# Kernel optimization log

Measured on AMD Instinct MI355X. Metric: run time of the kernel, lower is better.

Reference implementation:

```python
import jax, jax.numpy as jnp
import numpy as np

B, L, D, H = 2, 2048, 2048, 16
Dh = D // H
EPS = 1e-6
THETA = 500000.0


def _rope_cos_sin(dh, seq_len):
    # matches init_rope: per-head dim, theta=500000
    inv_freqs = 1.0 / (THETA ** (jnp.arange(0, dh, 2, dtype=jnp.float32) / dh))  # [Dh/2]
    t = jnp.arange(seq_len, dtype=jnp.float32)
    freqs = jnp.outer(t, inv_freqs)  # [L, Dh/2]
    return jnp.cos(freqs), jnp.sin(freqs)


def _apply_rope(x, cos, sin):
    # x: [B,L,H,Dh]; cos/sin: [L,Dh/2]
    xr = x.reshape(*x.shape[:-1], -1, 2)  # [B,L,H,Dh/2,2]
    c = cos[None, :, None, :]
    s = sin[None, :, None, :]
    rot = jnp.stack([xr[..., 0] * c - xr[..., 1] * s,
                     xr[..., 1] * c + xr[..., 0] * s], axis=-1)
    return rot.reshape(x.shape)


def setup_inputs() -> dict:
    key = jax.random.key(0)
    ks = jax.random.split(key, 5)
    std = 0.02
    x = jax.random.normal(ks[0], (B, L, D), dtype=jnp.float32)
    Wq = std * jax.random.normal(ks[1], (D, H, Dh), dtype=jnp.float32)
    Wk = std * jax.random.normal(ks[2], (D, H, Dh), dtype=jnp.float32)
    Wv = std * jax.random.normal(ks[3], (D, H, Dh), dtype=jnp.float32)
    Wout = (std / jnp.sqrt(2.0 * 24)) * jax.random.normal(ks[4], (D, D), dtype=jnp.float32)
    attn_scale = jnp.asarray(jnp.log2(float(L) ** 2 - float(L)), dtype=jnp.float32)
    return {"x": x, "Wq": Wq, "Wk": Wk, "Wv": Wv, "Wout": Wout, "attn_scale": attn_scale}


def reference(x, Wq, Wk, Wv, Wout, attn_scale):
    cos, sin = _rope_cos_sin(Dh, L)
    q = jnp.einsum('bld,dhk->blhk', x, Wq)  # [B,L,H,Dh]
    k = jnp.einsum('bld,dhk->blhk', x, Wk)
    v = jnp.einsum('bld,dhk->blhk', x, Wv)
    q = _apply_rope(q, cos, sin)
    k = _apply_rope(k, cos, sin)
    # QK L2 normalization
    q = q / (jnp.linalg.norm(q, axis=-1, keepdims=True) + EPS)
    k = k / (jnp.linalg.norm(k, axis=-1, keepdims=True) + EPS)
    att = jnp.einsum('bqhd,bkhd->bhqk', q, k)  # [B,H,L,L]
    mask = jnp.tril(jnp.ones((1, 1, L, L), dtype=jnp.bool_))
    neg_inf = jnp.finfo(jnp.float32).min
    att = jnp.where(mask, att, neg_inf)
    att = attn_scale * att
    att = jax.nn.softmax(att, axis=-1)
    out = jnp.einsum('bhqk,bkhd->bqhd', att, v)  # [B,L,H,Dh]
    out = out.reshape(B, L, D)
    return jnp.einsum('bld,de->ble', out, Wout)
```

## Files before the change

### kernel.cpp

```cpp
#include <hip/hip_runtime.h>
#include <hip/hip_fp16.h>

#define B_ 2
#define L_ 2048
#define D_ 2048
#define H_ 16
#define DH_ 128

typedef _Float16 f16;
typedef _Float16 f16x8 __attribute__((ext_vector_type(8)));
typedef _Float16 f16x4 __attribute__((ext_vector_type(4)));
typedef _Float16 f16x2 __attribute__((ext_vector_type(2)));
typedef float f32x4 __attribute__((ext_vector_type(4)));

__device__ __forceinline__ void gload_lds16(const void* g, void* l) {
  __builtin_amdgcn_global_load_lds(
      (__attribute__((address_space(1))) void*)(void*)g,
      (__attribute__((address_space(3))) void*)l, 16, 0, 0);
}

__device__ __forceinline__ float rmax16(float v) {
  v = fmaxf(v, __shfl_xor(v, 1));
  v = fmaxf(v, __shfl_xor(v, 2));
  v = fmaxf(v, __shfl_xor(v, 4));
  v = fmaxf(v, __shfl_xor(v, 8));
  return v;
}
__device__ __forceinline__ float rsum16(float v) {
  v += __shfl_xor(v, 1);
  v += __shfl_xor(v, 2);
  v += __shfl_xor(v, 4);
  v += __shfl_xor(v, 8);
  return v;
}

__global__ __launch_bounds__(256) void k_cast(const float* __restrict__ in,
                                              f16* __restrict__ out, int n8) {
  int i = blockIdx.x * blockDim.x + threadIdx.x;
  if (i >= n8) return;
  const float4* p = (const float4*)in + (size_t)i * 2;
  float4 a = p[0], b = p[1];
  f16x8 o;
  o[0] = (f16)a.x; o[1] = (f16)a.y; o[2] = (f16)a.z; o[3] = (f16)a.w;
  o[4] = (f16)b.x; o[5] = (f16)b.y; o[6] = (f16)b.z; o[7] = (f16)b.w;
  *((f16x8*)out + i) = o;
}

__global__ __launch_bounds__(256) void k_transpose4(
    const float* __restrict__ W0, const float* __restrict__ W1,
    const float* __restrict__ W2, const float* __restrict__ W3,
    f16* __restrict__ T0, f16* __restrict__ T1, f16* __restrict__ T2,
    f16* __restrict__ T3) {
  int z = blockIdx.z;
  const float* src = (z == 0) ? W0 : (z == 1) ? W1 : (z == 2) ? W2 : W3;
  f16* dst = (z == 0) ? T0 : (z == 1) ? T1 : (z == 2) ? T2 : T3;
  __shared__ float tile[32][33];
  int tx = threadIdx.x, ty = threadIdx.y;
  int x = blockIdx.x * 32 + tx;
  int y0 = blockIdx.y * 32;
#pragma unroll
  for (int i = 0; i < 4; ++i)
    tile[ty + i * 8][tx] = src[(size_t)(y0 + ty + i * 8) * 2048 + x];
  __syncthreads();
  int ox = y0 + tx;
  int oy0 = blockIdx.x * 32;
#pragma unroll
  for (int i = 0; i < 4; ++i)
    dst[(size_t)(oy0 + ty + i * 8) * 2048 + ox] = (f16)tile[tx][ty + i * 8];
}

__device__ __forceinline__ void gemm_core(const f16* __restrict__ A,
                                          const f16* __restrict__ BT,
                                          f16* As, f16* Bs, int m0, int n0,
                                          f32x4 (&acc)[4][4]) {
  const int tid = threadIdx.x;
  const int lane = tid & 63, w = tid >> 6;
  const int wr = w >> 1, wc = w & 1;
  const int li = lane & 15, lg = lane >> 4;
  for (int kt = 0; kt < 64; ++kt) {
    __syncthreads();
#pragma unroll
    for (int p = 0; p < 2; ++p) {
      int o = tid * 16 + p * 4096;
      int row = o >> 6, cb = o & 63;
      gload_lds16((const char*)A + (size_t)(m0 + row) * 4096 + kt * 64 + cb,
                  (char*)As + o);
      gload_lds16((const char*)BT + (size_t)(n0 + row) * 4096 + kt * 64 + cb,
                  (char*)Bs + o);
    }
    __syncthreads();
    f16x8 af[4], bf[4];
#pragma unroll
    for (int i = 0; i < 4; ++i) {
      af[i] = *(const f16x8*)(As + (wr * 64 + i * 16 + li) * 32 + lg * 8);
      bf[i] = *(const f16x8*)(Bs + (wc * 64 + i * 16 + li) * 32 + lg * 8);
    }
#pragma unroll
    for (int i = 0; i < 4; ++i)
#pragma unroll
      for (int j = 0; j < 4; ++j)
        acc[i][j] =
            __builtin_amdgcn_mfma_f32_16x16x32_f16(af[i], bf[j], acc[i][j], 0, 0, 0);
  }
}

__global__ __launch_bounds__(256) void k_gemm_qkv(
    const f16* __restrict__ x16, const f16* __restrict__ WqT,
    const f16* __restrict__ WkT, const f16* __restrict__ WvT,
    f16* __restrict__ qh, f16* __restrict__ kh, f16* __restrict__ vTo) {
  __shared__ alignas(16) f16 As[128 * 32];
  __shared__ alignas(16) f16 Bs[128 * 32];
  const int z = blockIdx.z;
  const f16* BT = (z == 0) ? WqT : (z == 1) ? WkT : WvT;
  const int m0 = blockIdx.y * 128, n0 = blockIdx.x * 128;
  f32x4 acc[4][4] = {};
  gemm_core(x16, BT, As, Bs, m0, n0, acc);
  const int lane = threadIdx.x & 63, w = threadIdx.x >> 6;
  const int wr = w >> 1, wc = w & 1, li = lane & 15, lg = lane >> 4;
  if (z < 2) {
    f16* out = (z == 0) ? qh : kh;
#pragma unroll
    for (int i = 0; i < 4; ++i) {
      int mb = m0 + wr * 64 + i * 16 + lg * 4;
#pragma unroll
      for (int j = 0; j < 4; ++j) {
        int n = n0 + wc * 64 + j * 16 + li;
        int h = n >> 7, dh = n & 127;
#pragma unroll
        for (int r = 0; r < 4; ++r) {
          int m = mb + r;
          int b = m >> 11, l = m & 2047;
          out[(((size_t)(b * 16 + h) * 2048 + l) << 7) + dh] = (f16)acc[i][j][r];
        }
      }
    }
  } else {
#pragma unroll
    for (int i = 0; i < 4; ++i) {
      int mb = m0 + wr * 64 + i * 16 + lg * 4;
      int b = mb >> 11, l = mb & 2047;
#pragma unroll
      for (int j = 0; j < 4; ++j) {
        int n = n0 + wc * 64 + j * 16 + li;
        int h = n >> 7, dh = n & 127;
        f16x4 v4;
#pragma unroll
        for (int r = 0; r < 4; ++r) v4[r] = (f16)acc[i][j][r];
        *(f16x4*)(vTo + ((size_t)(b * 16 + h) * 128 + dh) * 2048 + l) = v4;
      }
    }
  }
}

__global__ __launch_bounds__(256) void k_rope_norm(f16* __restrict__ qh,
                                                   f16* __restrict__ kh) {
  int gid = blockIdx.x * 4 + (threadIdx.x >> 6);
  int lane = threadIdx.x & 63;
  int which = gid >> 16;
  int r = gid & 65535;
  int l = r & 2047;
  f16* base = (which ? kh : qh) + (size_t)r * 128;
  f16x2 xv = *(f16x2*)(base + lane * 2);
  float x0 = (float)xv[0], x1 = (float)xv[1];
  float invf = exp2f(-(float)lane * 0.29580575889569f);
  float ang = (float)l * invf;
  float s, c;
  sincosf(ang, &s, &c);
  float y0 = x0 * c - x1 * s;
  float y1 = x1 * c + x0 * s;
  float ss = y0 * y0 + y1 * y1;
  ss += __shfl_xor(ss, 1);  ss += __shfl_xor(ss, 2);
  ss += __shfl_xor(ss, 4);  ss += __shfl_xor(ss, 8);
  ss += __shfl_xor(ss, 16); ss += __shfl_xor(ss, 32);
  float inv = 1.0f / (sqrtf(ss) + 1e-6f);
  f16x2 o;
  o[0] = (f16)(y0 * inv);
  o[1] = (f16)(y1 * inv);
  *(f16x2*)(base + lane * 2) = o;
}

__global__ __launch_bounds__(256) void k_flash(
    const f16* __restrict__ qh, const f16* __restrict__ kh,
    const f16* __restrict__ vT, f16* __restrict__ attO,
    const float* __restrict__ ascale_p) {
  const int bh = blockIdx.y;
  const int tid = threadIdx.x, lane = tid & 63, w = tid >> 6;
  const int li = lane & 15, lg = lane >> 4;
  const float csc = ascale_p[0] * 1.44269504088896f;
  const float thr = 8.0f / csc;

  __shared__ alignas(16) f16 Ks[64 * 136];
  __shared__ alignas(16) f16 Vs[128 * 72];
  __shared__ alignas(16) f16 Ps[4][16 * 72];

  const f16* qb = qh + (size_t)bh * 2048 * 128;
  const f16* kb = kh + (size_t)bh * 2048 * 128;
  const f16* vb = vT + (size_t)bh * 128 * 2048;
  const int b = bh >> 4, h = bh & 15;

#pragma unroll 1
  for (int ti = 0; ti < 2; ++ti) {
    const int t = ti ? (31 - (int)blockIdx.x) : (int)blockIdx.x;
    const int qw = t * 64 + w * 16;

    f16x8 Qr[4];
#pragma unroll
    for (int ks = 0; ks < 4; ++ks)
      Qr[ks] = *(const f16x8*)(qb + (size_t)(qw + li) * 128 + ks * 32 + lg * 8);

    f32x4 Oa[8] = {};
    float mrow[4], lrow[4];
#pragma unroll
    for (int r = 0; r < 4; ++r) { mrow[r] = -1e30f; lrow[r] = 0.0f; }

#pragma unroll 1
    for (int kt = 0; kt <= t; ++kt) {
      const int k0 = kt * 64;
      __syncthreads();
#pragma unroll
      for (int p = 0; p < 4; ++p) {
        int e = (p * 256 + tid) * 8;
        int row = e >> 7, col = e & 127;
        *(f16x8*)(Ks + row * 136 + col) =
            *(const f16x8*)(kb + (size_t)(k0 + row) * 128 + col);
        int row2 = e >> 6, col2 = e & 63;
        *(f16x8*)(Vs + row2 * 72 + col2) =
            *(const f16x8*)(vb + (size_t)row2 * 2048 + k0 + col2);
      }
      __syncthreads();

      f32x4 Sa[4] = {};
      __builtin_amdgcn_s_setprio(1);
#pragma unroll
      for (int ks = 0; ks < 4; ++ks) {
        f16x8 kf4[4];
#pragma unroll
        for (int kf = 0; kf < 4; ++kf)
          kf4[kf] = *(const f16x8*)(Ks + (kf * 16 + li) * 136 + ks * 32 + lg * 8);
#pragma unroll
        for (int kf = 0; kf < 4; ++kf)
          Sa[kf] = __builtin_amdgcn_mfma_f32_16x16x32_f16(Qr[ks], kf4[kf],
                                                          Sa[kf], 0, 0, 0);
      }
      __builtin_amdgcn_s_setprio(0);

      if (kt == t) {
#pragma unroll
        for (int kf = 0; kf < 4; ++kf)
#pragma unroll
          for (int r = 0; r < 4; ++r) {
            int qq = qw + lg * 4 + r;
            int kk = k0 + kf * 16 + li;
            if (kk > qq) Sa[kf][r] = -1e30f;
          }
      }

      float vmax[4];
      bool need = false;
#pragma unroll
      for (int r = 0; r < 4; ++r) {
        float v = fmaxf(fmaxf(Sa[0][r], Sa[1][r]), fmaxf(Sa[2][r], Sa[3][r]));
        v = rmax16(v);
        vmax[r] = v;
        need |= (v > mrow[r] + thr);
      }
      if (__any(need)) {
#pragma unroll
        for (int r = 0; r < 4; ++r) {
          float mnew = fmaxf(mrow[r], vmax[r]);
          float sc = exp2f(csc * (mrow[r] - mnew));
          mrow[r] = mnew;
          lrow[r] *= sc;
#pragma unroll
          for (int df = 0; df < 8; ++df) Oa[df][r] *= sc;
        }
      }
#pragma unroll
      for (int r = 0; r < 4; ++r) {
        float rs = 0.0f;
#pragma unroll
        for (int kf = 0; kf < 4; ++kf) {
          float p = exp2f(csc * (Sa[kf][r] - mrow[r]));
          Sa[kf][r] = p;
          rs += p;
        }
        rs = rsum16(rs);
        lrow[r] += rs;
      }

      f16* Pw = &Ps[w][0];
#pragma unroll
      for (int kf = 0; kf < 4; ++kf)
#pragma unroll
        for (int r = 0; r < 4; ++r)
          Pw[(lg * 4 + r) * 72 + kf * 16 + li] = (f16)Sa[kf][r];
      asm volatile("s_waitcnt lgkmcnt(0)" ::: "memory");
      __builtin_amdgcn_sched_barrier(0);
      __builtin_amdgcn_s_setprio(1);
#pragma unroll
      for (int k2 = 0; k2 < 2; ++k2) {
        f16x8 pa, vfr[8];
        pa = *(const f16x8*)(Pw + li * 72 + k2 * 32 + lg * 8);
#pragma unroll
        for (int df = 0; df < 8; ++df)
          vfr[df] = *(const f16x8*)(Vs + (df * 16 + li) * 72 + k2 * 32 + lg * 8);
#pragma unroll
        for (int df = 0; df < 8; ++df)
          Oa[df] = __builtin_amdgcn_mfma_f32_16x16x32_f16(pa, vfr[df],
                                                          Oa[df], 0, 0, 0);
      }
      __builtin_amdgcn_s_setprio(0);
    }

#pragma unroll
    for (int r = 0; r < 4; ++r) {
      float inv = 1.0f / lrow[r];
      int q = qw + lg * 4 + r;
      f16* orow = attO + (size_t)(b * 2048 + q) * 2048 + h * 128;
#pragma unroll
      for (int df = 0; df < 8; ++df)
        orow[df * 16 + li] = (f16)(Oa[df][r] * inv);
    }
  }
}

__global__ __launch_bounds__(256) void k_gemm_out(const f16* __restrict__ A,
                                                  const f16* __restrict__ WoutT,
                                                  float* __restrict__ out) {
  __shared__ alignas(16) f16 As[128 * 32];
  __shared__ alignas(16) f16 Bs[128 * 32];
  const int m0 = blockIdx.y * 128, n0 = blockIdx.x * 128;
  f32x4 acc[4][4] = {};
  gemm_core(A, WoutT, As, Bs, m0, n0, acc);
  const int lane = threadIdx.x & 63, w = threadIdx.x >> 6;
  const int wr = w >> 1, wc = w & 1, li = lane & 15, lg = lane >> 4;
#pragma unroll
  for (int i = 0; i < 4; ++i)
#pragma unroll
    for (int j = 0; j < 4; ++j) {
      int n = n0 + wc * 64 + j * 16 + li;
#pragma unroll
      for (int r = 0; r < 4; ++r) {
        int m = m0 + wr * 64 + i * 16 + lg * 4 + r;
        out[(size_t)m * 2048 + n] = acc[i][j][r];
      }
    }
}

extern "C" void kernel_launch(void* const* d_in, const int* in_sizes, int n_in,
                              void* d_out, int out_size, void* d_ws, size_t ws_size,
                              hipStream_t stream) {
  (void)in_sizes; (void)n_in; (void)out_size; (void)ws_size;
  const float* x = (const float*)d_in[0];
  const float* Wq = (const float*)d_in[1];
  const float* Wk = (const float*)d_in[2];
  const float* Wv = (const float*)d_in[3];
  const float* Wout = (const float*)d_in[4];
  const float* ascale = (const float*)d_in[5];

  char* ws = (char*)d_ws;
  f16* x16 = (f16*)(ws);
  f16* WoutT = (f16*)(ws + (16ull << 20));
  f16* WqT = (f16*)(ws + (24ull << 20));
  f16* WkT = (f16*)(ws + (32ull << 20));
  f16* WvT = (f16*)(ws + (40ull << 20));
  f16* qh = (f16*)(ws + (48ull << 20));
  f16* kh = (f16*)(ws + (64ull << 20));
  f16* vT = (f16*)(ws + (80ull << 20));
  f16* attO = (f16*)(ws + (24ull << 20));

  k_cast<<<dim3(4096), dim3(256), 0, stream>>>(x, x16, 1048576);
  k_transpose4<<<dim3(64, 64, 4), dim3(32, 8), 0, stream>>>(Wq, Wk, Wv, Wout,
                                                            WqT, WkT, WvT, WoutT);
  k_gemm_qkv<<<dim3(16, 32, 3), dim3(256), 0, stream>>>(x16, WqT, WkT, WvT, qh, kh, vT);
  k_rope_norm<<<dim3(32768), dim3(256), 0, stream>>>(qh, kh);
  k_flash<<<dim3(16, 32), dim3(256), 0, stream>>>(qh, kh, vT, attO, ascale);
  k_gemm_out<<<dim3(16, 32), dim3(256), 0, stream>>>(attO, WoutT, (float*)d_out);
}
```

Measured before the change: 441.6 us.

## Replace GEMM core with double-buffered 8-wave swizzled-LDS pipelined kernel

Both projection GEMMs move to a new 512-thread core with larger tiles (256x256 for QKV, 128x256 for the output projection) and a K-step of 64. It double-buffers LDS with XOR-swizzled layout and issues global-to-LDS prefetches interleaved with the MFMA phases. Waits use explicit vmcnt, and block indices are remapped to group tiles for cache locality. The goal is to hide global load latency, cut LDS bank conflicts and raise MFMA utilisation, at the cost of more registers and LDS, fewer blocks, and fragile hand-written wait counts.

```diff
diff --git a/kernel.cpp b/kernel.cpp
--- a/kernel.cpp
+++ b/kernel.cpp
@@ -17,6 +17,14 @@
   __builtin_amdgcn_global_load_lds(
       (__attribute__((address_space(1))) void*)(void*)g,
       (__attribute__((address_space(3))) void*)l, 16, 0, 0);
+}
+
+template <int N>
+__device__ __forceinline__ void waitcnt_vm() {
+  if constexpr (N == 0) asm volatile("s_waitcnt vmcnt(0)" ::: "memory");
+  else if constexpr (N == 4) asm volatile("s_waitcnt vmcnt(4)" ::: "memory");
+  else if constexpr (N == 6) asm volatile("s_waitcnt vmcnt(6)" ::: "memory");
+  else if constexpr (N == 8) asm volatile("s_waitcnt vmcnt(8)" ::: "memory");
 }
 
 __device__ __forceinline__ float rmax16(float v) {
@@ -69,84 +77,184 @@
     dst[(size_t)(oy0 + ty + i * 8) * 2048 + ox] = (f16)tile[tx][ty + i * 8];
 }
 
-__device__ __forceinline__ void gemm_core(const f16* __restrict__ A,
-                                          const f16* __restrict__ BT,
-                                          f16* As, f16* Bs, int m0, int n0,
-                                          f32x4 (&acc)[4][4]) {
+
+template <int NL>
+__device__ __forceinline__ void stage_slot(const char* __restrict__ src,
+                                           char* dst, int tid) {
+#pragma unroll
+  for (int j = 0; j < NL; ++j) {
+    int ci = j * 512 + tid;
+    int row = ci >> 3;
+    int sc = (ci & 7) ^ (row & 7);
+    gload_lds16(src + (size_t)row * 4096 + sc * 16, dst + ci * 16);
+  }
+}
+
+template <int BM>
+__device__ __forceinline__ void gemm8_core(const f16* __restrict__ A,
+                                           const f16* __restrict__ BT,
+                                           char* lds, int m0, int n0,
+                                           f32x4 (&acc)[BM / 32][4]) {
+  constexpr int WRS = BM / 2;
+  constexpr int MR = BM / 32;
+  constexpr int MPP = MR / 4;
+  constexpr int ALOADS = BM / 128;
+  constexpr int LPT = 2 * ALOADS + 4;
+  constexpr int ABYTES = BM * 128;
+  constexpr int BUFB = ABYTES + 32768;
+  constexpr int nt = 32;
+
   const int tid = threadIdx.x;
   const int lane = tid & 63, w = tid >> 6;
-  const int wr = w >> 1, wc = w & 1;
+  const int wr = w >> 2, wc = w & 3;
   const int li = lane & 15, lg = lane >> 4;
-  for (int kt = 0; kt < 64; ++kt) {
-    __syncthreads();
-#pragma unroll
-    for (int p = 0; p < 2; ++p) {
-      int o = tid * 16 + p * 4096;
-      int row = o >> 6, cb = o & 63;
-      gload_lds16((const char*)A + (size_t)(m0 + row) * 4096 + kt * 64 + cb,
-                  (char*)As + o);
-      gload_lds16((const char*)BT + (size_t)(n0 + row) * 4096 + kt * 64 + cb,
-                  (char*)Bs + o);
-    }
-    __syncthreads();
-    f16x8 af[4], bf[4];
-#pragma unroll
-    for (int i = 0; i < 4; ++i) {
-      af[i] = *(const f16x8*)(As + (wr * 64 + i * 16 + li) * 32 + lg * 8);
-      bf[i] = *(const f16x8*)(Bs + (wc * 64 + i * 16 + li) * 32 + lg * 8);
-    }
-#pragma unroll
-    for (int i = 0; i < 4; ++i)
-#pragma unroll
-      for (int j = 0; j < 4; ++j)
-        acc[i][j] =
-            __builtin_amdgcn_mfma_f32_16x16x32_f16(af[i], bf[j], acc[i][j], 0, 0, 0);
-  }
-}
-
-__global__ __launch_bounds__(256) void k_gemm_qkv(
+
+  const char* Ab = (const char*)A + (size_t)m0 * 4096;
+  const char* Bb = (const char*)BT + (size_t)n0 * 4096;
+
+  const int aoff0 = (wr * WRS + li) * 128 + ((lg) ^ (li & 7)) * 16;
+  const int aoff1 = (wr * WRS + li) * 128 + ((4 + lg) ^ (li & 7)) * 16;
+  const int boff0 = (wc * 64 + li) * 128 + ((lg) ^ (li & 7)) * 16;
+  const int boff1 = (wc * 64 + li) * 128 + ((4 + lg) ^ (li & 7)) * 16;
+
+#pragma unroll
+  for (int t = 0; t < 2; ++t) {
+    char* bA = lds + t * BUFB;
+    stage_slot<ALOADS>(Ab + t * 128, bA, tid);
+    stage_slot<ALOADS>(Ab + (size_t)WRS * 4096 + t * 128, bA + (size_t)WRS * 128, tid);
+    stage_slot<2>(Bb + t * 128, bA + ABYTES, tid);
+    stage_slot<2>(Bb + (size_t)128 * 4096 + t * 128, bA + ABYTES + 128 * 128, tid);
+  }
+  waitcnt_vm<LPT>();
+  __builtin_amdgcn_s_barrier();
+
+#pragma unroll 1
+  for (int u = 0; u < nt; ++u) {
+    const int c = u & 1;
+    char* bufA = lds + c * BUFB;
+    char* bufB = bufA + ABYTES;
+    char* oA = lds + (c ^ 1) * BUFB;
+    f16x8 bf[4][2];
+#pragma unroll
+    for (int p = 0; p < 4; ++p) {
+      f16x8 af[MPP][2];
+#pragma unroll
+      for (int i = 0; i < MPP; ++i) {
+        af[i][0] = *(const f16x8*)(bufA + aoff0 + (p * MPP + i) * 2048);
+        af[i][1] = *(const f16x8*)(bufA + aoff1 + (p * MPP + i) * 2048);
+      }
+      if (p == 0) {
+#pragma unroll
+        for (int nc = 0; nc < 4; ++nc) {
+          bf[nc][0] = *(const f16x8*)(bufB + boff0 + nc * 2048);
+          bf[nc][1] = *(const f16x8*)(bufB + boff1 + nc * 2048);
+        }
+      }
+      if (p == 0 && u >= 1 && u + 1 < nt)
+        stage_slot<ALOADS>(Ab + (size_t)(u + 1) * 128, oA, tid);
+      if (p == 1 && u >= 1 && u + 1 < nt)
+        stage_slot<ALOADS>(Ab + (size_t)WRS * 4096 + (size_t)(u + 1) * 128,
+                           oA + (size_t)WRS * 128, tid);
+      if (p == 2 && u + 2 < nt)
+        stage_slot<2>(Bb + (size_t)(u + 2) * 128, bufB, tid);
+      if (p == 3 && u + 2 < nt)
+        stage_slot<2>(Bb + (size_t)128 * 4096 + (size_t)(u + 2) * 128,
+                      bufB + 128 * 128, tid);
+      if (p == 3) {
+        if (u + 2 < nt) waitcnt_vm<4>();
+        else if (u + 1 < nt) waitcnt_vm<0>();
+      }
+      __builtin_amdgcn_s_barrier();
+      asm volatile("s_waitcnt lgkmcnt(0)" ::: "memory");
+      __builtin_amdgcn_sched_barrier(0);
+      __builtin_amdgcn_s_setprio(1);
+#pragma unroll
+      for (int i = 0; i < MPP; ++i)
+#pragma unroll
+        for (int nc = 0; nc < 4; ++nc) {
+          acc[p * MPP + i][nc] = __builtin_amdgcn_mfma_f32_16x16x32_f16(
+              af[i][0], bf[nc][0], acc[p * MPP + i][nc], 0, 0, 0);
+          acc[p * MPP + i][nc] = __builtin_amdgcn_mfma_f32_16x16x32_f16(
+              af[i][1], bf[nc][1], acc[p * MPP + i][nc], 0, 0, 0);
+        }
+      __builtin_amdgcn_s_setprio(0);
+      __builtin_amdgcn_s_barrier();
+    }
+  }
+}
+
+__global__ __launch_bounds__(512, 2) void k_gemm8_qkv(
     const f16* __restrict__ x16, const f16* __restrict__ WqT,
     const f16* __restrict__ WkT, const f16* __restrict__ WvT,
     f16* __restrict__ qh, f16* __restrict__ kh, f16* __restrict__ vTo) {
-  __shared__ alignas(16) f16 As[128 * 32];
-  __shared__ alignas(16) f16 Bs[128 * 32];
-  const int z = blockIdx.z;
+  __shared__ alignas(16) char lds[2 * (256 * 128 + 32768)];
+  const int pb = blockIdx.x;
+  const int lgc = (pb & 7) * 48 + (pb >> 3);
+  const int z = lgc >> 7;
+  const int r = lgc & 127;
+  const int m0 = (r >> 3) * 256, n0 = (r & 7) * 256;
   const f16* BT = (z == 0) ? WqT : (z == 1) ? WkT : WvT;
-  const int m0 = blockIdx.y * 128, n0 = blockIdx.x * 128;
-  f32x4 acc[4][4] = {};
-  gemm_core(x16, BT, As, Bs, m0, n0, acc);
+  f32x4 acc[8][4] = {};
+  gemm8_core<256>(x16, BT, lds, m0, n0, acc);
+
   const int lane = threadIdx.x & 63, w = threadIdx.x >> 6;
-  const int wr = w >> 1, wc = w & 1, li = lane & 15, lg = lane >> 4;
+  const int wr = w >> 2, wc = w & 3, li = lane & 15, lg = lane >> 4;
   if (z < 2) {
     f16* out = (z == 0) ? qh : kh;
 #pragma unroll
-    for (int i = 0; i < 4; ++i) {
-      int mb = m0 + wr * 64 + i * 16 + lg * 4;
-#pragma unroll
-      for (int j = 0; j < 4; ++j) {
-        int n = n0 + wc * 64 + j * 16 + li;
+    for (int mr = 0; mr < 8; ++mr) {
+      int mb = m0 + wr * 128 + mr * 16 + lg * 4;
+#pragma unroll
+      for (int nc = 0; nc < 4; ++nc) {
+        int n = n0 + wc * 64 + nc * 16 + li;
         int h = n >> 7, dh = n & 127;
 #pragma unroll
-        for (int r = 0; r < 4; ++r) {
-          int m = mb + r;
+        for (int r2 = 0; r2 < 4; ++r2) {
+          int m = mb + r2;
           int b = m >> 11, l = m & 2047;
-          out[(((size_t)(b * 16 + h) * 2048 + l) << 7) + dh] = (f16)acc[i][j][r];
+          out[(((size_t)(b * 16 + h) * 2048 + l) << 7) + dh] = (f16)acc[mr][nc][r2];
         }
       }
     }
   } else {
 #pragma unroll
-    for (int i = 0; i < 4; ++i) {
-      int mb = m0 + wr * 64 + i * 16 + lg * 4;
+    for (int mr = 0; mr < 8; ++mr) {
+      int mb = m0 + wr * 128 + mr * 16 + lg * 4;
       int b = mb >> 11, l = mb & 2047;
 #pragma unroll
-      for (int j = 0; j < 4; ++j) {
-        int n = n0 + wc * 64 + j * 16 + li;
+      for (int nc = 0; nc < 4; ++nc) {
+        int n = n0 + wc * 64 + nc * 16 + li;
         int h = n >> 7, dh = n & 127;
         f16x4 v4;
 #pragma unroll
-        for (int r = 0; r < 4; ++r) v4[r] = (f16)acc[i][j][r];
+        for (int r2 = 0; r2 < 4; ++r2) v4[r2] = (f16)acc[mr][nc][r2];
         *(f16x4*)(vTo + ((size_t)(b * 16 + h) * 128 + dh) * 2048 + l) = v4;
+      }
+    }
+  }
+}
+
+__global__ __launch_bounds__(512, 2) void k_gemm8_out(
+    const f16* __restrict__ A, const f16* __restrict__ WoutT,
+    float* __restrict__ out) {
+  __shared__ alignas(16) char lds[2 * (128 * 128 + 32768)];
+  const int pb = blockIdx.x;
+  const int lgc = (pb & 7) * 32 + (pb >> 3);
+  const int m0 = (lgc >> 3) * 128, n0 = (lgc & 7) * 256;
+  f32x4 acc[4][4] = {};
+  gemm8_core<128>(A, WoutT, lds, m0, n0, acc);
+
+  const int lane = threadIdx.x & 63, w = threadIdx.x >> 6;
+  const int wr = w >> 2, wc = w & 3, li = lane & 15, lg = lane >> 4;
+#pragma unroll
+  for (int mr = 0; mr < 4; ++mr) {
+#pragma unroll
+    for (int nc = 0; nc < 4; ++nc) {
+      int n = n0 + wc * 64 + nc * 16 + li;
+#pragma unroll
+      for (int r2 = 0; r2 < 4; ++r2) {
+        int m = m0 + wr * 64 + mr * 16 + lg * 4 + r2;
+        out[(size_t)m * 2048 + n] = acc[mr][nc][r2];
       }
     }
   }
@@ -324,29 +432,6 @@
   }
 }
 
-__global__ __launch_bounds__(256) void k_gemm_out(const f16* __restrict__ A,
-                                                  const f16* __restrict__ WoutT,
-                                                  float* __restrict__ out) {
-  __shared__ alignas(16) f16 As[128 * 32];
-  __shared__ alignas(16) f16 Bs[128 * 32];
-  const int m0 = blockIdx.y * 128, n0 = blockIdx.x * 128;
-  f32x4 acc[4][4] = {};
-  gemm_core(A, WoutT, As, Bs, m0, n0, acc);
-  const int lane = threadIdx.x & 63, w = threadIdx.x >> 6;
-  const int wr = w >> 1, wc = w & 1, li = lane & 15, lg = lane >> 4;
-#pragma unroll
-  for (int i = 0; i < 4; ++i)
-#pragma unroll
-    for (int j = 0; j < 4; ++j) {
-      int n = n0 + wc * 64 + j * 16 + li;
-#pragma unroll
-      for (int r = 0; r < 4; ++r) {
-        int m = m0 + wr * 64 + i * 16 + lg * 4 + r;
-        out[(size_t)m * 2048 + n] = acc[i][j][r];
-      }
-    }
-}
-
 extern "C" void kernel_launch(void* const* d_in, const int* in_sizes, int n_in,
                               void* d_out, int out_size, void* d_ws, size_t ws_size,
                               hipStream_t stream) {
@@ -372,8 +457,8 @@
   k_cast<<<dim3(4096), dim3(256), 0, stream>>>(x, x16, 1048576);
   k_transpose4<<<dim3(64, 64, 4), dim3(32, 8), 0, stream>>>(Wq, Wk, Wv, Wout,
                                                             WqT, WkT, WvT, WoutT);
-  k_gemm_qkv<<<dim3(16, 32, 3), dim3(256), 0, stream>>>(x16, WqT, WkT, WvT, qh, kh, vT);
+  k_gemm8_qkv<<<dim3(384), dim3(512), 0, stream>>>(x16, WqT, WkT, WvT, qh, kh, vT);
   k_rope_norm<<<dim3(32768), dim3(256), 0, stream>>>(qh, kh);
   k_flash<<<dim3(16, 32), dim3(256), 0, stream>>>(qh, kh, vT, attO, ascale);
-  k_gemm_out<<<dim3(16, 32), dim3(256), 0, stream>>>(attO, WoutT, (float*)d_out);
-}
+  k_gemm8_out<<<dim3(256), dim3(512), 0, stream>>>(attO, WoutT, (float*)d_out);
+}
```

After: 435.6 us. About the same (-1.3%).
